# Optimization experiments

Measured on AMD Instinct MI355X. Metric: run time of the kernel, lower is better.

The kernel has to match this reference:

```python
import jax, jax.numpy as jnp
import numpy as np

N_NODES = 10000
N_FEATS = 128
BSZ = 32
D = 100000


def setup_inputs() -> dict:
    key = jax.random.key(0)
    k_vals, k_idx = jax.random.split(key)
    flat_inputs = jax.random.normal(k_vals, (BSZ, D), dtype=jnp.float32)
    # Sample D UNIQUE (node, feat) slots per batch row so the scatter has no
    # duplicate destinations (torch duplicate writes are nondeterministic).
    n_slots = N_NODES * N_FEATS
    keys = jax.random.split(k_idx, BSZ)
    flat_pos = jax.vmap(lambda k: jax.random.permutation(k, n_slots)[:D])(keys)  # [BSZ, D]
    node_ids = (flat_pos // N_FEATS).astype(jnp.int64)
    feat_ids = (flat_pos % N_FEATS).astype(jnp.int64)
    return {"flat_inputs": flat_inputs, "node_ids": node_ids, "feat_ids": feat_ids}


def reference(flat_inputs, node_ids, feat_ids):
    bsz, d = flat_inputs.shape
    # Linearize (batch, node, feat) -> single flat index; one fused scatter.
    batch_ids = jnp.arange(bsz, dtype=node_ids.dtype)[:, None]  # [bsz, 1] broadcasts over D
    lin = (batch_ids * N_NODES + node_ids) * N_FEATS + feat_ids  # [bsz, D]
    obs_mat = jnp.zeros((bsz * N_NODES * N_FEATS,), dtype=flat_inputs.dtype)
    obs_mat = obs_mat.at[lin.reshape(-1)].set(flat_inputs.reshape(-1), unique_indices=True)
    return obs_mat.reshape(bsz, N_NODES, N_FEATS)
```

## Files before the change

### kernel.cpp

```cpp
#include <hip/hip_runtime.h>
#include <stdint.h>

#define N_NODES 10000
#define N_FEATS 128
#define BSZ 32
#define D_ELEMS 100000

#define OUT_ELEMS (BSZ * N_NODES * N_FEATS)
#define N_ITEMS   (BSZ * D_ELEMS)
#define N_GROUPS  (N_ITEMS / 4)

#define NBUCKET 512
#define CHUNK   (OUT_ELEMS / NBUCKET)
#define CAP     8064
#define SUBF    16000
#define NSUB    (CHUNK / SUBF)

typedef float f32x4 __attribute__((ext_vector_type(4)));
typedef int   i32x4 __attribute__((ext_vector_type(4)));

__global__ __launch_bounds__(512) void bin_kernel(
    const f32x4* __restrict__ vals,
    const i32x4* __restrict__ nodes,
    const i32x4* __restrict__ feats,
    uint64_t* __restrict__ pairs,
    uint32_t* __restrict__ gcount) {
  __shared__ uint32_t hist[NBUCKET];
  __shared__ uint32_t base_s[NBUCKET];
  const int tid = threadIdx.x;
  hist[tid] = 0;
  __syncthreads();

  const int gbase = blockIdx.x * 2048;
  uint32_t lin[16];
  float    val[16];
  uint32_t rnk[16];

#pragma unroll
  for (int k = 0; k < 4; ++k) {
    int g = gbase + k * 512 + tid;
    bool a = (g < N_GROUPS);
    int gg = a ? g : 0;
    f32x4 v = vals[gg];
    i32x4 n = nodes[gg];
    i32x4 f = feats[gg];
    uint32_t rowbase = (uint32_t)((gg * 4) / D_ELEMS) * (uint32_t)(N_NODES * N_FEATS);
    lin[k*4+0] = a ? rowbase + (uint32_t)n.x * N_FEATS + (uint32_t)f.x : 0xFFFFFFFFu;
    lin[k*4+1] = a ? rowbase + (uint32_t)n.y * N_FEATS + (uint32_t)f.y : 0xFFFFFFFFu;
    lin[k*4+2] = a ? rowbase + (uint32_t)n.z * N_FEATS + (uint32_t)f.z : 0xFFFFFFFFu;
    lin[k*4+3] = a ? rowbase + (uint32_t)n.w * N_FEATS + (uint32_t)f.w : 0xFFFFFFFFu;
    val[k*4+0] = v.x; val[k*4+1] = v.y; val[k*4+2] = v.z; val[k*4+3] = v.w;
  }

#pragma unroll
  for (int i = 0; i < 16; ++i)
    if (lin[i] != 0xFFFFFFFFu)
      rnk[i] = atomicAdd(&hist[lin[i] / CHUNK], 1u);
  __syncthreads();

  {
    uint32_t h = hist[tid];
    base_s[tid] = h ? atomicAdd(&gcount[tid], h) : 0u;
  }
  __syncthreads();

#pragma unroll
  for (int i = 0; i < 16; ++i) {
    if (lin[i] != 0xFFFFFFFFu) {
      uint32_t bkt = lin[i] / CHUNK;
      uint32_t slot = base_s[bkt] + rnk[i];
      if (slot < CAP)
        pairs[(size_t)bkt * CAP + slot] =
            ((uint64_t)__float_as_uint(val[i]) << 32) | (uint64_t)lin[i];
    }
  }
}

__global__ __launch_bounds__(1024) void expand_kernel(
    const uint64_t* __restrict__ pairs,
    const uint32_t* __restrict__ gcount,
    float* __restrict__ out) {
  __shared__ float chunk[SUBF];
  const int b = blockIdx.x;
  const int tid = threadIdx.x;
  uint32_t cnt = gcount[b];
  if (cnt > CAP) cnt = CAP;

  uint32_t ml[8];
  float    mv[8];
  const uint64_t* bp = pairs + (size_t)b * CAP;
  const uint32_t cbase = (uint32_t)(b * CHUNK);
#pragma unroll
  for (int i = 0; i < 8; ++i) {
    uint32_t idx = (uint32_t)tid + (uint32_t)i * 1024u;
    uint64_t p = (idx < cnt) ? bp[idx] : ~0ull;
    ml[i] = (uint32_t)p - cbase;
    mv[i] = __uint_as_float((uint32_t)(p >> 32));
  }

  f32x4* c4 = (f32x4*)chunk;
  const f32x4 z = {0.f, 0.f, 0.f, 0.f};
#pragma unroll
  for (int j = 0; j < 4; ++j) {
    int idx = tid + j * 1024;
    if (idx < SUBF / 4) c4[idx] = z;
  }
  __syncthreads();

  const size_t outbase = (size_t)b * CHUNK;
  for (int p = 0; p < NSUB; ++p) {
    uint32_t lo = (uint32_t)(p * SUBF);
#pragma unroll
    for (int i = 0; i < 8; ++i) {
      uint32_t loc = ml[i] - lo;
      if (loc < SUBF) chunk[loc] = mv[i];
    }
    __syncthreads();
    f32x4* o4 = (f32x4*)(out + outbase + lo);
#pragma unroll
    for (int j = 0; j < 4; ++j) {
      int idx = tid + j * 1024;
      if (idx < SUBF / 4) {
        f32x4 v = c4[idx];
        c4[idx] = z;
        o4[idx] = v;
      }
    }
    __syncthreads();
  }
}

__global__ __launch_bounds__(256) void scatter4_kernel(
    const f32x4* __restrict__ vals,
    const i32x4* __restrict__ node_ids,
    const i32x4* __restrict__ feat_ids,
    float* __restrict__ out) {
  int t = blockIdx.x * blockDim.x + threadIdx.x;
  if (t >= N_GROUPS) return;
  int b = (t * 4) / D_ELEMS;
  f32x4 v = vals[t];
  i32x4 n = node_ids[t];
  i32x4 f = feat_ids[t];
  size_t base = (size_t)b * N_NODES * N_FEATS;
  out[base + (size_t)n.x * N_FEATS + (size_t)f.x] = v.x;
  out[base + (size_t)n.y * N_FEATS + (size_t)f.y] = v.y;
  out[base + (size_t)n.z * N_FEATS + (size_t)f.z] = v.z;
  out[base + (size_t)n.w * N_FEATS + (size_t)f.w] = v.w;
}

extern "C" void kernel_launch(void* const* d_in, const int* in_sizes, int n_in,
                              void* d_out, int out_size, void* d_ws, size_t ws_size,
                              hipStream_t stream) {
  const float* vals     = (const float*)d_in[0];
  const int*   node_ids = (const int*)d_in[1];
  const int*   feat_ids = (const int*)d_in[2];
  float* out = (float*)d_out;

  const size_t pairs_bytes = (size_t)NBUCKET * CAP * sizeof(uint64_t);
  const size_t need = pairs_bytes + NBUCKET * sizeof(uint32_t);

  if (ws_size >= need) {
    uint64_t* pairs  = (uint64_t*)d_ws;
    uint32_t* gcount = (uint32_t*)((char*)d_ws + pairs_bytes);
    hipMemsetAsync(gcount, 0, NBUCKET * sizeof(uint32_t), stream);
    const int grid1 = (N_GROUPS + 2047) / 2048;
    bin_kernel<<<grid1, 512, 0, stream>>>(
        (const f32x4*)vals, (const i32x4*)node_ids, (const i32x4*)feat_ids,
        pairs, gcount);
    expand_kernel<<<NBUCKET, 1024, 0, stream>>>(pairs, gcount, out);
  } else {
    hipMemsetAsync(out, 0, (size_t)out_size * sizeof(float), stream);
    const int grid = (N_GROUPS + 255) / 256;
    scatter4_kernel<<<grid, 256, 0, stream>>>(
        (const f32x4*)vals, (const i32x4*)node_ids, (const i32x4*)feat_ids, out);
  }
}
```

Measured before the change: 50.59 us.

## Replace global bucket atomics with per-block sorted runs and directory lookup

The binning kernel now sorts each block's pairs by bucket in shared memory and writes them contiguously, along with a per-block offset directory. This removes the global atomic counters and their memset. The expand kernel scans the directory column for its bucket and binary-searches the owning block to gather its pairs. Output stores become nontemporal. The cost is extra scans and binary searches, more synchronisation, and gathers from up to 800 separate runs.

```diff
diff --git a/kernel.cpp b/kernel.cpp
--- a/kernel.cpp
+++ b/kernel.cpp
@@ -12,91 +12,148 @@
 
 #define NBUCKET 512
 #define CHUNK   (OUT_ELEMS / NBUCKET)
-#define CAP     8064
 #define SUBF    16000
 #define NSUB    (CHUNK / SUBF)
 
+#define GPB   1024
+#define IPB   (GPB * 4)
+#define NBLK  ((N_GROUPS + GPB - 1) / GPB)
+#define DIRP  800
+#define MAXP  8192
+
 typedef float f32x4 __attribute__((ext_vector_type(4)));
 typedef int   i32x4 __attribute__((ext_vector_type(4)));
+typedef unsigned long long u64x2 __attribute__((ext_vector_type(2)));
 
 __global__ __launch_bounds__(512) void bin_kernel(
     const f32x4* __restrict__ vals,
     const i32x4* __restrict__ nodes,
     const i32x4* __restrict__ feats,
     uint64_t* __restrict__ pairs,
-    uint32_t* __restrict__ gcount) {
+    uint16_t* __restrict__ dir) {
   __shared__ uint32_t hist[NBUCKET];
-  __shared__ uint32_t base_s[NBUCKET];
+  __shared__ uint32_t sincl[NBUCKET];
+  __shared__ uint32_t excl[NBUCKET];
+  __shared__ alignas(16) uint64_t sp[IPB];
   const int tid = threadIdx.x;
+  const int blk = blockIdx.x;
   hist[tid] = 0;
   __syncthreads();
 
-  const int gbase = blockIdx.x * 2048;
-  uint32_t lin[16];
-  float    val[16];
-  uint32_t rnk[16];
-
-#pragma unroll
-  for (int k = 0; k < 4; ++k) {
-    int g = gbase + k * 512 + tid;
+  uint32_t lin[8]; float val[8]; uint32_t rnk[8]; uint32_t bkt[8];
+  const int gbase = blk * GPB;
+#pragma unroll
+  for (int q = 0; q < 2; ++q) {
+    int g = gbase + q * 512 + tid;
     bool a = (g < N_GROUPS);
     int gg = a ? g : 0;
     f32x4 v = vals[gg];
     i32x4 n = nodes[gg];
     i32x4 f = feats[gg];
     uint32_t rowbase = (uint32_t)((gg * 4) / D_ELEMS) * (uint32_t)(N_NODES * N_FEATS);
-    lin[k*4+0] = a ? rowbase + (uint32_t)n.x * N_FEATS + (uint32_t)f.x : 0xFFFFFFFFu;
-    lin[k*4+1] = a ? rowbase + (uint32_t)n.y * N_FEATS + (uint32_t)f.y : 0xFFFFFFFFu;
-    lin[k*4+2] = a ? rowbase + (uint32_t)n.z * N_FEATS + (uint32_t)f.z : 0xFFFFFFFFu;
-    lin[k*4+3] = a ? rowbase + (uint32_t)n.w * N_FEATS + (uint32_t)f.w : 0xFFFFFFFFu;
-    val[k*4+0] = v.x; val[k*4+1] = v.y; val[k*4+2] = v.z; val[k*4+3] = v.w;
-  }
-
-#pragma unroll
-  for (int i = 0; i < 16; ++i)
+    lin[q*4+0] = a ? rowbase + (uint32_t)n.x * N_FEATS + (uint32_t)f.x : 0xFFFFFFFFu;
+    lin[q*4+1] = a ? rowbase + (uint32_t)n.y * N_FEATS + (uint32_t)f.y : 0xFFFFFFFFu;
+    lin[q*4+2] = a ? rowbase + (uint32_t)n.z * N_FEATS + (uint32_t)f.z : 0xFFFFFFFFu;
+    lin[q*4+3] = a ? rowbase + (uint32_t)n.w * N_FEATS + (uint32_t)f.w : 0xFFFFFFFFu;
+    val[q*4+0] = v.x; val[q*4+1] = v.y; val[q*4+2] = v.z; val[q*4+3] = v.w;
+  }
+
+#pragma unroll
+  for (int i = 0; i < 8; ++i) {
+    bkt[i] = lin[i] / CHUNK;
     if (lin[i] != 0xFFFFFFFFu)
-      rnk[i] = atomicAdd(&hist[lin[i] / CHUNK], 1u);
-  __syncthreads();
-
-  {
-    uint32_t h = hist[tid];
-    base_s[tid] = h ? atomicAdd(&gcount[tid], h) : 0u;
-  }
-  __syncthreads();
-
-#pragma unroll
-  for (int i = 0; i < 16; ++i) {
+      rnk[i] = atomicAdd(&hist[bkt[i]], 1u);
+  }
+  __syncthreads();
+
+  sincl[tid] = hist[tid];
+  __syncthreads();
+  for (int s = 1; s < NBUCKET; s <<= 1) {
+    uint32_t v = sincl[tid];
+    if (tid >= s) v += sincl[tid - s];
+    __syncthreads();
+    sincl[tid] = v;
+    __syncthreads();
+  }
+  excl[tid] = sincl[tid] - hist[tid];
+  uint32_t tot = sincl[NBUCKET - 1];
+  __syncthreads();
+
+#pragma unroll
+  for (int i = 0; i < 8; ++i) {
     if (lin[i] != 0xFFFFFFFFu) {
-      uint32_t bkt = lin[i] / CHUNK;
-      uint32_t slot = base_s[bkt] + rnk[i];
-      if (slot < CAP)
-        pairs[(size_t)bkt * CAP + slot] =
-            ((uint64_t)__float_as_uint(val[i]) << 32) | (uint64_t)lin[i];
-    }
-  }
+      uint32_t slot = excl[bkt[i]] + rnk[i];
+      sp[slot] = ((uint64_t)__float_as_uint(val[i]) << 32) | (uint64_t)lin[i];
+    }
+  }
+  __syncthreads();
+
+  const u64x2* sp2 = (const u64x2*)sp;
+  u64x2* gp2 = (u64x2*)(pairs + (size_t)blk * IPB);
+  uint32_t tot2 = (tot + 1u) >> 1;
+  for (uint32_t i = tid; i < tot2; i += 512u) gp2[i] = sp2[i];
+
+  dir[(uint32_t)tid * DIRP + (uint32_t)blk] = (uint16_t)excl[tid];
+  if (tid == 0)
+    dir[(uint32_t)NBUCKET * DIRP + (uint32_t)blk] = (uint16_t)tot;
 }
 
 __global__ __launch_bounds__(1024) void expand_kernel(
     const uint64_t* __restrict__ pairs,
-    const uint32_t* __restrict__ gcount,
+    const uint16_t* __restrict__ dir,
     float* __restrict__ out) {
   __shared__ float chunk[SUBF];
   const int b = blockIdx.x;
   const int tid = threadIdx.x;
-  uint32_t cnt = gcount[b];
-  if (cnt > CAP) cnt = CAP;
-
-  uint32_t ml[8];
-  float    mv[8];
-  const uint64_t* bp = pairs + (size_t)b * CAP;
+  uint32_t* w = (uint32_t*)chunk;
+  uint32_t* S = w;
+  uint32_t* P = w + 1024;
+
+  uint32_t d0 = 0, cntk = 0;
+  if (tid < NBLK) {
+    d0 = dir[(uint32_t)b * DIRP + (uint32_t)tid];
+    uint32_t d1 = dir[(uint32_t)(b + 1) * DIRP + (uint32_t)tid];
+    cntk = d1 - d0;
+  }
+  S[tid] = (uint32_t)tid * IPB + d0;
+  P[tid] = cntk;
+  __syncthreads();
+
+  for (int s = 1; s < 1024; s <<= 1) {
+    uint32_t v = P[tid];
+    if (tid >= s) v += P[tid - s];
+    __syncthreads();
+    P[tid] = v;
+    __syncthreads();
+  }
+  uint32_t total = P[1023];
+  uint32_t ex = P[tid] - cntk;
+  __syncthreads();
+  P[tid] = ex;
+  __syncthreads();
+  uint32_t cnt = total > MAXP ? MAXP : total;
+
+  uint32_t ml[8]; float mv[8];
   const uint32_t cbase = (uint32_t)(b * CHUNK);
 #pragma unroll
-  for (int i = 0; i < 8; ++i) {
-    uint32_t idx = (uint32_t)tid + (uint32_t)i * 1024u;
-    uint64_t p = (idx < cnt) ? bp[idx] : ~0ull;
-    ml[i] = (uint32_t)p - cbase;
-    mv[i] = __uint_as_float((uint32_t)(p >> 32));
-  }
+  for (int j = 0; j < 8; ++j) {
+    uint32_t i = (uint32_t)tid + (uint32_t)j * 1024u;
+    uint32_t l = 0xFFFFFFFFu; float v = 0.f;
+    if (i < cnt) {
+      int k = 0;
+#pragma unroll
+      for (int s = 512; s > 0; s >>= 1) {
+        int t = k + s;
+        if (t < 1024 && P[t] <= i) k = t;
+      }
+      uint64_t p = pairs[(size_t)S[k] + (size_t)(i - P[k])];
+      l = (uint32_t)p;
+      v = __uint_as_float((uint32_t)(p >> 32));
+    }
+    ml[j] = l - cbase;
+    mv[j] = v;
+  }
+  __syncthreads();
 
   f32x4* c4 = (f32x4*)chunk;
   const f32x4 z = {0.f, 0.f, 0.f, 0.f};
@@ -123,7 +180,7 @@
       if (idx < SUBF / 4) {
         f32x4 v = c4[idx];
         c4[idx] = z;
-        o4[idx] = v;
+        __builtin_nontemporal_store(v, &o4[idx]);
       }
     }
     __syncthreads();
@@ -156,18 +213,17 @@
   const int*   feat_ids = (const int*)d_in[2];
   float* out = (float*)d_out;
 
-  const size_t pairs_bytes = (size_t)NBUCKET * CAP * sizeof(uint64_t);
-  const size_t need = pairs_bytes + NBUCKET * sizeof(uint32_t);
+  const size_t pairs_bytes = (size_t)NBLK * IPB * sizeof(uint64_t);
+  const size_t dir_bytes   = (size_t)(NBUCKET + 1) * DIRP * sizeof(uint16_t);
+  const size_t need = pairs_bytes + dir_bytes;
 
   if (ws_size >= need) {
-    uint64_t* pairs  = (uint64_t*)d_ws;
-    uint32_t* gcount = (uint32_t*)((char*)d_ws + pairs_bytes);
-    hipMemsetAsync(gcount, 0, NBUCKET * sizeof(uint32_t), stream);
-    const int grid1 = (N_GROUPS + 2047) / 2048;
-    bin_kernel<<<grid1, 512, 0, stream>>>(
+    uint64_t* pairs = (uint64_t*)d_ws;
+    uint16_t* dir   = (uint16_t*)((char*)d_ws + pairs_bytes);
+    bin_kernel<<<NBLK, 512, 0, stream>>>(
         (const f32x4*)vals, (const i32x4*)node_ids, (const i32x4*)feat_ids,
-        pairs, gcount);
-    expand_kernel<<<NBUCKET, 1024, 0, stream>>>(pairs, gcount, out);
+        pairs, dir);
+    expand_kernel<<<NBUCKET, 1024, 0, stream>>>(pairs, dir, out);
   } else {
     hipMemsetAsync(out, 0, (size_t)out_size * sizeof(float), stream);
     const int grid = (N_GROUPS + 255) / 256;
```

Result: slower. 55.20 us (+9.1%).

## Stage binned pairs in shared memory for bucket-ordered coalesced writes

Applied to the files above, without the earlier changes.

The bin kernel now computes an in-block exclusive prefix sum over the bucket histogram and first places each pair into a bucket-sorted shared-memory array. It then writes the pairs out in sorted order, so consecutive threads write adjacent slots of the same bucket region instead of scattering 8-byte stores randomly. To fit the 32 KB staging buffer, each block handles half as many items, which doubles the block count and the number of global gcount atomics. The aim is better write coalescing in exchange for an extra shared-memory pass and more synchronisation.

```diff
diff --git a/kernel.cpp b/kernel.cpp
--- a/kernel.cpp
+++ b/kernel.cpp
@@ -15,6 +15,10 @@
 #define CAP     8064
 #define SUBF    16000
 #define NSUB    (CHUNK / SUBF)
+
+#define BIN_GPB   1024
+#define BIN_IPB   (BIN_GPB * 4)
+#define BIN_NBLK  ((N_GROUPS + BIN_GPB - 1) / BIN_GPB)
 
 typedef float f32x4 __attribute__((ext_vector_type(4)));
 typedef int   i32x4 __attribute__((ext_vector_type(4)));
@@ -26,53 +30,82 @@
     uint64_t* __restrict__ pairs,
     uint32_t* __restrict__ gcount) {
   __shared__ uint32_t hist[NBUCKET];
+  __shared__ uint32_t excl[NBUCKET];
   __shared__ uint32_t base_s[NBUCKET];
+  __shared__ uint32_t wpart[8];
+  __shared__ uint32_t tot_s;
+  __shared__ alignas(16) uint64_t sp[BIN_IPB];
   const int tid = threadIdx.x;
   hist[tid] = 0;
   __syncthreads();
 
-  const int gbase = blockIdx.x * 2048;
-  uint32_t lin[16];
-  float    val[16];
-  uint32_t rnk[16];
-
-#pragma unroll
-  for (int k = 0; k < 4; ++k) {
-    int g = gbase + k * 512 + tid;
+  uint32_t lin[8]; float val[8]; uint32_t rnk[8];
+  const int gbase = blockIdx.x * BIN_GPB;
+#pragma unroll
+  for (int q = 0; q < 2; ++q) {
+    int g = gbase + q * 512 + tid;
     bool a = (g < N_GROUPS);
     int gg = a ? g : 0;
     f32x4 v = vals[gg];
     i32x4 n = nodes[gg];
     i32x4 f = feats[gg];
     uint32_t rowbase = (uint32_t)((gg * 4) / D_ELEMS) * (uint32_t)(N_NODES * N_FEATS);
-    lin[k*4+0] = a ? rowbase + (uint32_t)n.x * N_FEATS + (uint32_t)f.x : 0xFFFFFFFFu;
-    lin[k*4+1] = a ? rowbase + (uint32_t)n.y * N_FEATS + (uint32_t)f.y : 0xFFFFFFFFu;
-    lin[k*4+2] = a ? rowbase + (uint32_t)n.z * N_FEATS + (uint32_t)f.z : 0xFFFFFFFFu;
-    lin[k*4+3] = a ? rowbase + (uint32_t)n.w * N_FEATS + (uint32_t)f.w : 0xFFFFFFFFu;
-    val[k*4+0] = v.x; val[k*4+1] = v.y; val[k*4+2] = v.z; val[k*4+3] = v.w;
-  }
-
-#pragma unroll
-  for (int i = 0; i < 16; ++i)
+    lin[q*4+0] = a ? rowbase + (uint32_t)n.x * N_FEATS + (uint32_t)f.x : 0xFFFFFFFFu;
+    lin[q*4+1] = a ? rowbase + (uint32_t)n.y * N_FEATS + (uint32_t)f.y : 0xFFFFFFFFu;
+    lin[q*4+2] = a ? rowbase + (uint32_t)n.z * N_FEATS + (uint32_t)f.z : 0xFFFFFFFFu;
+    lin[q*4+3] = a ? rowbase + (uint32_t)n.w * N_FEATS + (uint32_t)f.w : 0xFFFFFFFFu;
+    val[q*4+0] = v.x; val[q*4+1] = v.y; val[q*4+2] = v.z; val[q*4+3] = v.w;
+  }
+
+#pragma unroll
+  for (int i = 0; i < 8; ++i)
     if (lin[i] != 0xFFFFFFFFu)
       rnk[i] = atomicAdd(&hist[lin[i] / CHUNK], 1u);
   __syncthreads();
 
-  {
-    uint32_t h = hist[tid];
-    base_s[tid] = h ? atomicAdd(&gcount[tid], h) : 0u;
-  }
-  __syncthreads();
-
-#pragma unroll
-  for (int i = 0; i < 16; ++i) {
+  uint32_t h = hist[tid];
+  uint32_t v = h;
+#pragma unroll
+  for (int s = 1; s < 64; s <<= 1) {
+    uint32_t u = __shfl_up(v, s, 64);
+    if ((tid & 63) >= s) v += u;
+  }
+  if ((tid & 63) == 63) wpart[tid >> 6] = v;
+  __syncthreads();
+  if (tid < 64) {
+    uint32_t p = (tid < 8) ? wpart[tid] : 0u;
+#pragma unroll
+    for (int s = 1; s < 8; s <<= 1) {
+      uint32_t u = __shfl_up(p, s, 64);
+      if (tid >= s) p += u;
+    }
+    if (tid < 8) wpart[tid] = p;
+  }
+  __syncthreads();
+  uint32_t woff = (tid >= 64) ? wpart[(tid >> 6) - 1] : 0u;
+  uint32_t incl = v + woff;
+  excl[tid] = incl - h;
+  base_s[tid] = h ? atomicAdd(&gcount[tid], h) : 0u;
+  if (tid == 511) tot_s = incl;
+  __syncthreads();
+
+#pragma unroll
+  for (int i = 0; i < 8; ++i) {
     if (lin[i] != 0xFFFFFFFFu) {
-      uint32_t bkt = lin[i] / CHUNK;
-      uint32_t slot = base_s[bkt] + rnk[i];
-      if (slot < CAP)
-        pairs[(size_t)bkt * CAP + slot] =
-            ((uint64_t)__float_as_uint(val[i]) << 32) | (uint64_t)lin[i];
-    }
+      uint32_t b = lin[i] / CHUNK;
+      sp[excl[b] + rnk[i]] =
+          ((uint64_t)__float_as_uint(val[i]) << 32) | (uint64_t)lin[i];
+    }
+  }
+  __syncthreads();
+
+  const uint32_t tot = tot_s;
+  for (uint32_t i = tid; i < tot; i += 512u) {
+    uint64_t p = sp[i];
+    uint32_t l = (uint32_t)p;
+    uint32_t b = l / CHUNK;
+    uint32_t dst = base_s[b] + (i - excl[b]);
+    if (dst < CAP) pairs[(size_t)b * CAP + dst] = p;
   }
 }
 
@@ -163,8 +196,7 @@
     uint64_t* pairs  = (uint64_t*)d_ws;
     uint32_t* gcount = (uint32_t*)((char*)d_ws + pairs_bytes);
     hipMemsetAsync(gcount, 0, NBUCKET * sizeof(uint32_t), stream);
-    const int grid1 = (N_GROUPS + 2047) / 2048;
-    bin_kernel<<<grid1, 512, 0, stream>>>(
+    bin_kernel<<<BIN_NBLK, 512, 0, stream>>>(
         (const f32x4*)vals, (const i32x4*)node_ids, (const i32x4*)feat_ids,
         pairs, gcount);
     expand_kernel<<<NBUCKET, 1024, 0, stream>>>(pairs, gcount, out);
```

Result: faster. 49.01 us, median of 2 (-3.1%).
